# Optimization experiments

Hardware: AMD Instinct MI355X
Metric: run time of the kernel (lower is better)

## Reference

```python
import jax, jax.numpy as jnp
import numpy as np


def setup_inputs() -> dict:
    key = jax.random.key(0)
    ks = jax.random.split(key, 8)
    B, T, H, Hu = 128, 64, 1024, 512
    MJW = 64                    # max_jump_width
    J = 2 * MJW + 1             # size_jump_width_set_nn = 129
    N = 2 * T                   # HMM states (word states + null states)
    I = 64                      # source sentence length
    sc = 0.02
    return {
        "y_hidden": jax.random.normal(ks[0], (B, T, H), jnp.float32),
        # emission probs p(source word i | state s), strictly positive for log
        "emission": jax.random.uniform(ks[1], (B, N, I), jnp.float32, 1e-4, 1.0),
        "source_lengths": jax.random.randint(ks[2], (B,), 1, I + 1),
        "W1": jax.random.normal(ks[3], (H, Hu), jnp.float32) * sc,
        "b1": jnp.zeros((Hu,), jnp.float32),
        "W2": jax.random.normal(ks[4], (Hu, J), jnp.float32) * sc,
        "b2": jnp.zeros((J,), jnp.float32),
        "W3": jax.random.normal(ks[5], (Hu, 1), jnp.float32) * sc,
        "b3": jnp.zeros((1,), jnp.float32),
        "max_jump_width": MJW,
    }


def _build_transition(y_hidden, W1, b1, W2, b2, W3, b3, mjw):
    # Dense(tanh) -> Dense softmax jump-width distribution + Dense sigmoid p0
    B, T, _ = y_hidden.shape
    ts = jnp.tanh(y_hidden @ W1 + b1)                       # [B,T,Hu]
    jw = jax.nn.softmax(ts @ W2 + b2, axis=-1)              # [B,T,J]
    p0 = jax.nn.sigmoid(jnp.squeeze(ts @ W3 + b3, -1))      # [B,T]
    r = jnp.arange(T)
    # banded gather: transition[i, j] = jw[i, mjw + j - i]
    band_idx = mjw + r[None, :] - r[:, None]                # [T,T], in [0, J)
    band = jnp.take_along_axis(jw, band_idx[None], axis=2)  # [B,T,T]
    diag_p0 = jnp.eye(T, dtype=jw.dtype) * p0[:, :, None]   # [B,T,T]
    top = jnp.concatenate([band, diag_p0], axis=2)          # [B,T,2T]
    return jnp.concatenate([top, top], axis=1)              # [B,2T,2T]


def _forward_alignment(transition, emission, source_lengths):
    # Faithful translation of the tf.scan forward algorithm. tf.scan with no
    # initializer uses elems[0] as the initial accumulator and emits it as
    # output[0] (log part = ones, so the [0,0] element is 1.0).
    B, N, I = emission.shape
    em = jnp.transpose(emission, (2, 0, 1))                 # [I,B,N]
    alpha0 = jnp.broadcast_to(em[0][:, None, :], (B, N, N)) # rows all equal e_0
    L0 = jnp.ones((B,), emission.dtype)

    def step(carry, e):
        alpha, L = carry                                    # [B,N,N], [B]
        yi = e[:, None, :]                                  # rows of yi_prob identical
        m1 = jnp.matmul(alpha, transition)                  # [B,N,N]
        tmp = m1 * yi
        tmp = tmp / jnp.sum(tmp, axis=2, keepdims=True)     # row-normalized alpha
        m2 = jnp.matmul(transition, alpha) * yi             # [B,N,N]
        max_j = jnp.max(m2, axis=-1)[:, 0]                  # gather row 0 -> [B]
        state_prev = jnp.sum(m1, axis=1)                    # [B,N]
        state = jnp.log(e) + jnp.log(state_prev) - max_j[:, None]
        state_log = jnp.log(jnp.sum(jnp.exp(state), axis=-1))
        L_new = L + state_log + max_j                       # [B]
        return (tmp, L_new), L_new

    (_, _), logs = jax.lax.scan(step, (alpha0, L0), em[1:])  # [I-1,B]
    logs = jnp.concatenate([L0[None], logs], axis=0).T       # [B,I]
    idx = (source_lengths - 1)[:, None]
    return jnp.take_along_axis(logs, idx, axis=1)[:, 0]      # [B]


def reference(y_hidden, emission, source_lengths, W1, b1, W2, b2, W3, b3, max_jump_width):
    transition = _build_transition(y_hidden, W1, b1, W2, b2, W3, b3, max_jump_width)
    return _forward_alignment(transition, emission, source_lengths)
```

## Files before the change

kernel.cpp:

```cpp
#include <hip/hip_runtime.h>
#include <hip/hip_bf16.h>

typedef float f32x4 __attribute__((ext_vector_type(4)));
typedef __bf16 bf16x8 __attribute__((ext_vector_type(8)));
typedef unsigned short u16;

#define OFF_W1T  0u
#define OFF_W23B 1048576u
#define OFF_TS   1196032u
#define OFF_JWT  9584640u
#define OFF_P0   11681792u

static __device__ __forceinline__ u16 f2bf(float x) {
    __bf16 h = (__bf16)x;
    return __builtin_bit_cast(u16, h);
}

__device__ __forceinline__ void gload16(const void* g, void* l) {
    __builtin_amdgcn_global_load_lds(
        (const __attribute__((address_space(1))) void*)g,
        (__attribute__((address_space(3))) void*)l,
        16, 0, 0);
}

__global__ __launch_bounds__(256) void prep_kernel(
    const float* __restrict__ W1, const float* __restrict__ W2,
    const float* __restrict__ W3,
    __bf16* __restrict__ W1T, __bf16* __restrict__ W23B)
{
    const int t = threadIdx.x;
    if (blockIdx.x < 128) {
        __shared__ __bf16 lds_t[64][72];
        const int kt = blockIdx.x >> 3, nt = blockIdx.x & 7;
        const int k0 = kt * 64, n0 = nt * 64;
        {
            const int kr = t >> 2, c0 = (t & 3) * 16;
            const float* src = W1 + (size_t)(k0 + kr) * 512 + n0 + c0;
            #pragma unroll
            for (int q = 0; q < 4; ++q) {
                float4 v = *(const float4*)(src + q * 4);
                lds_t[kr][c0 + q * 4 + 0] = (__bf16)v.x;
                lds_t[kr][c0 + q * 4 + 1] = (__bf16)v.y;
                lds_t[kr][c0 + q * 4 + 2] = (__bf16)v.z;
                lds_t[kr][c0 + q * 4 + 3] = (__bf16)v.w;
            }
        }
        __syncthreads();
        {
            const int nr = t >> 2, kc = (t & 3) * 16;
            bf16x8 o0, o1;
            #pragma unroll
            for (int j = 0; j < 8; ++j) o0[j] = lds_t[kc + j][nr];
            #pragma unroll
            for (int j = 0; j < 8; ++j) o1[j] = lds_t[kc + 8 + j][nr];
            __bf16* dst = W1T + (size_t)(n0 + nr) * 1024 + k0 + kc;
            *(bf16x8*)(dst)     = o0;
            *(bf16x8*)(dst + 8) = o1;
        }
    } else {
        int g = (blockIdx.x - 128) * 256 + t;
        if (g < 9216) {
            int n = g >> 6;
            int k8 = (g & 63) * 8;
            bf16x8 v;
            #pragma unroll
            for (int j = 0; j < 8; ++j) {
                int k = k8 + j;
                float x = 0.0f;
                if (n < 129) x = W2[(size_t)k * 129 + n];
                else if (n == 129) x = W3[k];
                v[j] = (__bf16)x;
            }
            int kk = k8 >> 5, lg = (k8 >> 3) & 3, ct = n >> 4, lr = n & 15;
            *(bf16x8*)&W23B[(((size_t)(kk * 9 + ct)) * 64 + lg * 16 + lr) * 8] = v;
        }
    }
}

__global__ __launch_bounds__(256, 3) void gemm1_kernel(
    const float* __restrict__ Y, const __bf16* __restrict__ W1T,
    const float* __restrict__ b1, u16* __restrict__ ts)
{
    __shared__ float  As[3][64 * 32];
    __shared__ __bf16 Bs[3][128 * 32];
    const int tid = threadIdx.x;
    const int bid = blockIdx.x;
    const int half = bid >> 8;
    const int b8 = bid & 255;
    const int xcd = b8 & 7;
    const int ii = b8 >> 3;
    const int rb = half * 64 + xcd * 8 + (ii >> 2);
    const int tb = ii & 3;
    const int m0 = rb * 64, n0 = tb * 128;
    const int wid = tid >> 6, lane = tid & 63;
    const int wr = wid >> 1, wc = wid & 1;
    const int lr = lane & 15, lg = lane >> 4;
    const int al = lane >> 3;
    const int au = (lane & 7) ^ al;
    const float* yA0 = Y + (size_t)(m0 + (wid * 2 + 0) * 8 + al) * 1024 + au * 4;
    const float* yA1 = Y + (size_t)(m0 + (wid * 2 + 1) * 8 + al) * 1024 + au * 4;
    const int bl = lane >> 2;
    const int bu = (lane & 3) ^ ((bl >> 1) & 3);
    const __bf16* wB0 = W1T + (size_t)(n0 + (wid * 2 + 0) * 16 + bl) * 1024 + bu * 8;
    const __bf16* wB1 = W1T + (size_t)(n0 + (wid * 2 + 1) * 16 + bl) * 1024 + bu * 8;

    f32x4 acc[2][4];
    #pragma unroll
    for (int m = 0; m < 2; m++)
        #pragma unroll
        for (int n = 0; n < 4; n++) { f32x4 z = {0.f,0.f,0.f,0.f}; acc[m][n] = z; }

#define STAGE(buf, kt) do { \
    gload16(yA0 + (kt) * 32, &As[buf][(wid * 2 + 0) * 256]); \
    gload16(yA1 + (kt) * 32, &As[buf][(wid * 2 + 1) * 256]); \
    gload16(wB0 + (kt) * 32, &Bs[buf][(wid * 2 + 0) * 512]); \
    gload16(wB1 + (kt) * 32, &Bs[buf][(wid * 2 + 1) * 512]); \
} while (0)

#define COMPUTE(buf) do { \
    bf16x8 af[2]; bf16x8 bfr[4]; \
    _Pragma("unroll") \
    for (int m = 0; m < 2; ++m) { \
        const int row = wr * 32 + m * 16 + lr; \
        const int r7 = row & 7; \
        float4 h0 = *(const float4*)&As[buf][row * 32 + (((lg * 2 + 0) ^ r7) * 4)]; \
        float4 h1 = *(const float4*)&As[buf][row * 32 + (((lg * 2 + 1) ^ r7) * 4)]; \
        bf16x8 tt; \
        tt[0]=(__bf16)h0.x; tt[1]=(__bf16)h0.y; tt[2]=(__bf16)h0.z; tt[3]=(__bf16)h0.w; \
        tt[4]=(__bf16)h1.x; tt[5]=(__bf16)h1.y; tt[6]=(__bf16)h1.z; tt[7]=(__bf16)h1.w; \
        af[m] = tt; \
    } \
    _Pragma("unroll") \
    for (int n = 0; n < 4; ++n) { \
        const int rowb = wc * 64 + n * 16 + lr; \
        bfr[n] = *(const bf16x8*)&Bs[buf][rowb * 32 + ((lg ^ ((rowb >> 1) & 3)) * 8)]; \
    } \
    __builtin_amdgcn_s_setprio(1); \
    _Pragma("unroll") \
    for (int m = 0; m < 2; ++m) \
        _Pragma("unroll") \
        for (int n = 0; n < 4; ++n) \
            acc[m][n] = __builtin_amdgcn_mfma_f32_16x16x32_bf16(af[m], bfr[n], acc[m][n], 0, 0, 0); \
    __builtin_amdgcn_s_setprio(0); \
} while (0)

    STAGE(0, 0); STAGE(1, 1);
    {
        int buf = 0, sbuf = 2;
        #pragma unroll 1
        for (int kt = 0; kt < 30; ++kt) {
            asm volatile("s_waitcnt vmcnt(4)" ::: "memory");
            __builtin_amdgcn_s_barrier();
            COMPUTE(buf);
            STAGE(sbuf, kt + 2);
            buf  = (buf  == 2) ? 0 : buf  + 1;
            sbuf = (sbuf == 2) ? 0 : sbuf + 1;
        }
    }
    asm volatile("s_waitcnt vmcnt(4)" ::: "memory");
    __builtin_amdgcn_s_barrier();
    COMPUTE(0);
    asm volatile("s_waitcnt vmcnt(0)" ::: "memory");
    __builtin_amdgcn_s_barrier();
    COMPUTE(1);

    #pragma unroll
    for (int m = 0; m < 2; m++) {
        #pragma unroll
        for (int n = 0; n < 4; n++) {
            int col = n0 + wc * 64 + n * 16 + lr;
            float bias = b1[col];
            #pragma unroll
            for (int j = 0; j < 4; j++) {
                int row = m0 + wr * 32 + m * 16 + lg * 4 + j;
                float v = tanhf(acc[m][n][j] + bias);
                ts[(size_t)row * 512 + col] = f2bf(v);
            }
        }
    }
#undef STAGE
#undef COMPUTE
}

__global__ __launch_bounds__(256) void band_kernel(
    const u16* __restrict__ ts, const u16* __restrict__ W23B,
    const float* __restrict__ b2, const float* __restrict__ b3,
    float* __restrict__ jwT, float* __restrict__ p0)
{
    const int b = blockIdx.x;
    const int tid = threadIdx.x;
    const int w = tid >> 6, lane = tid & 63;
    const int lr = lane & 15, lg = lane >> 4;
    const int r0 = b * 64 + w * 16;

    f32x4 acc[9];
    #pragma unroll
    for (int ct = 0; ct < 9; ct++) { f32x4 z = {0.f,0.f,0.f,0.f}; acc[ct] = z; }

    #pragma unroll 4
    for (int kk = 0; kk < 16; ++kk) {
        bf16x8 a = *(const bf16x8*)(ts + (size_t)(r0 + lr) * 512 + kk * 32 + lg * 8);
        #pragma unroll
        for (int ct = 0; ct < 9; ct++) {
            bf16x8 bv = *(const bf16x8*)(W23B + ((size_t)(kk * 9 + ct) * 64 + lane) * 8);
            acc[ct] = __builtin_amdgcn_mfma_f32_16x16x32_bf16(a, bv, acc[ct], 0, 0, 0);
        }
    }

    float b3v = b3[0];
    #pragma unroll
    for (int j = 0; j < 4; j++) {
        int rloc = w * 16 + lg * 4 + j;
        float v[9];
        float mx = -1e30f;
        #pragma unroll
        for (int ct = 0; ct < 9; ct++) {
            int col = ct * 16 + lr;
            if (col < 129) { float x = acc[ct][j] + b2[col]; v[ct] = x; mx = fmaxf(mx, x); }
            else v[ct] = -1e30f;
        }
        #pragma unroll
        for (int o = 1; o < 16; o <<= 1) mx = fmaxf(mx, __shfl_xor(mx, o));
        float sum = 0.f;
        #pragma unroll
        for (int ct = 0; ct < 9; ct++) {
            int col = ct * 16 + lr;
            if (col < 129) { float e = expf(v[ct] - mx); v[ct] = e; sum += e; }
        }
        #pragma unroll
        for (int o = 1; o < 16; o <<= 1) sum += __shfl_xor(sum, o);
        float inv = 1.0f / sum;
        #pragma unroll
        for (int ct = 0; ct < 9; ct++) {
            int col = ct * 16 + lr;
            int cc = col - 64 + rloc;
            if (col < 129 && cc >= 0 && cc < 64)
                jwT[((size_t)b * 64 + cc) * 64 + rloc] = v[ct] * inv;
        }
        if (lr == 1) {
            float pv = acc[8][j] + b3v;
            p0[b * 64 + rloc] = 1.0f / (1.0f + expf(-pv));
        }
    }
}

__global__ __launch_bounds__(64, 1) void recur_kernel(
    const float* __restrict__ jwT, const float* __restrict__ p0g,
    const float* __restrict__ em, const int* __restrict__ slen,
    float* __restrict__ out)
{
    __shared__ float em_s[128][65];
    __shared__ f32x4 a_bc4[16];
    const int b = blockIdx.x, c = threadIdx.x;

    const float* bb = jwT + ((size_t)b * 64 + c) * 64;
    f32x4 B0  = *(const f32x4*)(bb + 0);
    f32x4 B1  = *(const f32x4*)(bb + 4);
    f32x4 B2  = *(const f32x4*)(bb + 8);
    f32x4 B3  = *(const f32x4*)(bb + 12);
    f32x4 B4  = *(const f32x4*)(bb + 16);
    f32x4 B5  = *(const f32x4*)(bb + 20);
    f32x4 B6  = *(const f32x4*)(bb + 24);
    f32x4 B7  = *(const f32x4*)(bb + 28);
    f32x4 B8  = *(const f32x4*)(bb + 32);
    f32x4 B9  = *(const f32x4*)(bb + 36);
    f32x4 B10 = *(const f32x4*)(bb + 40);
    f32x4 B11 = *(const f32x4*)(bb + 44);
    f32x4 B12 = *(const f32x4*)(bb + 48);
    f32x4 B13 = *(const f32x4*)(bb + 52);
    f32x4 B14 = *(const f32x4*)(bb + 56);
    f32x4 B15 = *(const f32x4*)(bb + 60);

    {
        const float4* eg = (const float4*)(em + (size_t)b * 8192);
        #pragma unroll 8
        for (int q = 0; q < 32; ++q) {
            int i4 = c + q * 64;
            float4 v = eg[i4];
            int base = i4 * 4; int n = base >> 6; int ii = base & 63;
            em_s[n][ii] = v.x; em_s[n][ii + 1] = v.y; em_s[n][ii + 2] = v.z; em_s[n][ii + 3] = v.w;
        }
    }
    const float p0r = p0g[b * 64 + c];
    const int idx = slen[b] - 1;
    __syncthreads();

    float ut = em_s[c][0] + em_s[c + 64][0];
    int Eacc = 0;

    unsigned rbase = (unsigned)(uintptr_t)(__attribute__((address_space(3))) void*)&a_bc4[0];
    unsigned waddr = rbase + (unsigned)c * 4u;
    unsigned emlo_base = (unsigned)(uintptr_t)(__attribute__((address_space(3))) void*)&em_s[c][0];
    unsigned emhi_base = (unsigned)(uintptr_t)(__attribute__((address_space(3))) void*)&em_s[c + 64][0];

    float em_lo = em_s[c][1];
    float em_hi = em_s[c + 64][1];

    #pragma unroll 1
    for (int i = 1; i <= idx; ++i) {
        unsigned ealo = emlo_base + (unsigned)((i + 1) * 4);
        unsigned eahi = emhi_base + (unsigned)((i + 1) * 4);
        f32x4 A0,A1,A2,A3,A4,A5,A6,A7,A8,A9,A10,A11,A12,A13,A14,A15;
        float nlo, nhi;
        asm volatile(
            "ds_write_b32 %19, %18\n\t"
            "ds_read_b128 %0, %20 offset:0\n\t"
            "ds_read_b128 %1, %20 offset:16\n\t"
            "ds_read_b128 %2, %20 offset:32\n\t"
            "ds_read_b128 %3, %20 offset:48\n\t"
            "ds_read_b128 %4, %20 offset:64\n\t"
            "ds_read_b128 %5, %20 offset:80\n\t"
            "ds_read_b128 %6, %20 offset:96\n\t"
            "ds_read_b128 %7, %20 offset:112\n\t"
            "ds_read_b128 %8, %20 offset:128\n\t"
            "ds_read_b128 %9, %20 offset:144\n\t"
            "ds_read_b128 %10, %20 offset:160\n\t"
            "ds_read_b128 %11, %20 offset:176\n\t"
            "ds_read_b128 %12, %20 offset:192\n\t"
            "ds_read_b128 %13, %20 offset:208\n\t"
            "ds_read_b128 %14, %20 offset:224\n\t"
            "ds_read_b128 %15, %20 offset:240\n\t"
            "ds_read_b32 %16, %21\n\t"
            "ds_read_b32 %17, %22"
            : "=&v"(A0), "=&v"(A1), "=&v"(A2),  "=&v"(A3),
              "=&v"(A4), "=&v"(A5), "=&v"(A6),  "=&v"(A7),
              "=&v"(A8), "=&v"(A9), "=&v"(A10), "=&v"(A11),
              "=&v"(A12),"=&v"(A13),"=&v"(A14), "=&v"(A15),
              "=&v"(nlo), "=&v"(nhi)
            : "v"(ut), "v"(waddr), "v"(rbase), "v"(ealo), "v"(eahi)
            : "memory");
        int bits = __builtin_amdgcn_readfirstlane(__float_as_int(ut));
        int ef = (bits >> 23) & 255;
        Eacc += ef - 127;
        float scale = __int_as_float((254 - ef) << 23);
        float emlo_eff = em_lo * scale;
        float emhi_eff = em_hi * p0r * scale;
        asm volatile("s_waitcnt lgkmcnt(0)" ::: "memory");
        __builtin_amdgcn_sched_barrier(0);
        f32x4 va = A0 * B0;
        f32x4 vb = A1 * B1;
        f32x4 vc = A2 * B2;
        f32x4 vd = A3 * B3;
        va = va + A4 * B4;   vb = vb + A5 * B5;
        vc = vc + A6 * B6;   vd = vd + A7 * B7;
        va = va + A8 * B8;   vb = vb + A9 * B9;
        vc = vc + A10 * B10; vd = vd + A11 * B11;
        va = va + A12 * B12; vb = vb + A13 * B13;
        vc = vc + A14 * B14; vd = vd + A15 * B15;
        f32x4 vs = (va + vb) + (vc + vd);
        float sum = (vs[0] + vs[1]) + (vs[2] + vs[3]);
        ut = sum * emlo_eff + ut * emhi_eff;
        em_lo = nlo; em_hi = nhi;
    }
    float r = ut;
    #pragma unroll
    for (int o = 1; o < 64; o <<= 1) r += __shfl_xor(r, o);
    if (c == 0) {
        float res = 1.0f;
        if (idx > 0)
            res = 1.0f + 0.6931471805599453f * ((float)Eacc + __log2f(r) + 7.0f * (float)idx);
        out[b] = res;
    }
}

extern "C" void kernel_launch(void* const* d_in, const int* in_sizes, int n_in,
                              void* d_out, int out_size, void* d_ws, size_t ws_size,
                              hipStream_t stream)
{
    const float* Y   = (const float*)d_in[0];
    const float* em  = (const float*)d_in[1];
    const int*   sl  = (const int*)d_in[2];
    const float* W1  = (const float*)d_in[3];
    const float* b1  = (const float*)d_in[4];
    const float* W2  = (const float*)d_in[5];
    const float* b2  = (const float*)d_in[6];
    const float* W3  = (const float*)d_in[7];
    const float* b3  = (const float*)d_in[8];
    float* out = (float*)d_out;
    char* ws = (char*)d_ws;

    __bf16* W1T  = (__bf16*)(ws + OFF_W1T);
    __bf16* W23B = (__bf16*)(ws + OFF_W23B);
    u16*    ts   = (u16*)(ws + OFF_TS);
    float*  jwT  = (float*)(ws + OFF_JWT);
    float*  p0   = (float*)(ws + OFF_P0);

    prep_kernel<<<164, 256, 0, stream>>>(W1, W2, W3, W1T, W23B);
    gemm1_kernel<<<512, 256, 0, stream>>>(Y, W1T, b1, ts);
    band_kernel<<<128, 256, 0, stream>>>(ts, (const u16*)W23B, b2, b3, jwT, p0);
    recur_kernel<<<128, 64, 0, stream>>>(jwT, p0, em, sl, out);
}
```

Before: 76.17 us.

## Replace sequential vector recurrence with bf16 MFMA matrix-product scan

The per-batch recurrence kernel, which walked a 64-element state vector through idx serial matvec steps on one wavefront, is replaced by a 256-thread kernel. This kernel accumulates the product of per-step 64x64 transition matrices with bf16 MFMA, using swizzled LDS tiles and max-based exponent rescaling. The final vector is applied once at the end. The aim is to use matrix cores and four waves in place of a latency-bound single-wave loop, but each step now does a full matrix-matrix product plus a block barrier. Keeping the products in bf16 also risks losing accuracy.

```diff
diff --git a/kernel.cpp b/kernel.cpp
--- a/kernel.cpp
+++ b/kernel.cpp
@@ -3,6 +3,7 @@
 
 typedef float f32x4 __attribute__((ext_vector_type(4)));
 typedef __bf16 bf16x8 __attribute__((ext_vector_type(8)));
+typedef __bf16 bf16x4 __attribute__((ext_vector_type(4)));
 typedef unsigned short u16;
 
 #define OFF_W1T  0u
@@ -244,122 +245,167 @@
     }
 }
 
-__global__ __launch_bounds__(64, 1) void recur_kernel(
+__global__ __launch_bounds__(256, 1) void scan_kernel(
     const float* __restrict__ jwT, const float* __restrict__ p0g,
     const float* __restrict__ em, const int* __restrict__ slen,
     float* __restrict__ out)
 {
-    __shared__ float em_s[128][65];
-    __shared__ f32x4 a_bc4[16];
-    const int b = blockIdx.x, c = threadIdx.x;
-
-    const float* bb = jwT + ((size_t)b * 64 + c) * 64;
-    f32x4 B0  = *(const f32x4*)(bb + 0);
-    f32x4 B1  = *(const f32x4*)(bb + 4);
-    f32x4 B2  = *(const f32x4*)(bb + 8);
-    f32x4 B3  = *(const f32x4*)(bb + 12);
-    f32x4 B4  = *(const f32x4*)(bb + 16);
-    f32x4 B5  = *(const f32x4*)(bb + 20);
-    f32x4 B6  = *(const f32x4*)(bb + 24);
-    f32x4 B7  = *(const f32x4*)(bb + 28);
-    f32x4 B8  = *(const f32x4*)(bb + 32);
-    f32x4 B9  = *(const f32x4*)(bb + 36);
-    f32x4 B10 = *(const f32x4*)(bb + 40);
-    f32x4 B11 = *(const f32x4*)(bb + 44);
-    f32x4 B12 = *(const f32x4*)(bb + 48);
-    f32x4 B13 = *(const f32x4*)(bb + 52);
-    f32x4 B14 = *(const f32x4*)(bb + 56);
-    f32x4 B15 = *(const f32x4*)(bb + 60);
+    __shared__ __bf16 Mb[64 * 64];
+    __shared__ __bf16 PT[2][64 * 64];
+    __shared__ float  emT[64][132];
+    __shared__ float  p0s[64];
+    __shared__ float  wmax[2][4];
+    __shared__ float  partial[4][64];
+
+    const int b = blockIdx.x;
+    const int t = threadIdx.x;
+    const int w = t >> 6, lane = t & 63;
+    const int lr = lane & 15, lg = lane >> 4;
+    const int idx = slen[b] - 1;
+
+    if (idx <= 0) { if (t == 0) out[b] = 1.0f; return; }
 
     {
-        const float4* eg = (const float4*)(em + (size_t)b * 8192);
-        #pragma unroll 8
-        for (int q = 0; q < 32; ++q) {
-            int i4 = c + q * 64;
-            float4 v = eg[i4];
-            int base = i4 * 4; int n = base >> 6; int ii = base & 63;
-            em_s[n][ii] = v.x; em_s[n][ii + 1] = v.y; em_s[n][ii + 2] = v.z; em_s[n][ii + 3] = v.w;
-        }
-    }
-    const float p0r = p0g[b * 64 + c];
-    const int idx = slen[b] - 1;
+        const float4* mg4 = (const float4*)(jwT + (size_t)b * 4096);
+        #pragma unroll
+        for (int q = 0; q < 4; ++q) {
+            int i4 = t + q * 256;
+            float4 v = mg4[i4];
+            int m = i4 >> 4, k0 = (i4 & 15) * 4;
+            int u = (k0 >> 3) ^ (m & 7);
+            bf16x4 o; o[0]=(__bf16)v.x; o[1]=(__bf16)v.y; o[2]=(__bf16)v.z; o[3]=(__bf16)v.w;
+            *(bf16x4*)&Mb[m * 64 + u * 8 + (k0 & 7)] = o;
+        }
+        const float4* eg4 = (const float4*)(em + (size_t)b * 8192);
+        #pragma unroll
+        for (int q = 0; q < 8; ++q) {
+            int i4 = t + q * 256;
+            float4 v = eg4[i4];
+            int n = i4 >> 4, i0 = (i4 & 15) * 4;
+            emT[i0 + 0][n] = v.x;
+            emT[i0 + 1][n] = v.y;
+            emT[i0 + 2][n] = v.z;
+            emT[i0 + 3][n] = v.w;
+        }
+        if (t < 64) p0s[t] = p0g[b * 64 + t];
+    }
     __syncthreads();
 
-    float ut = em_s[c][0] + em_s[c + 64][0];
+    const int m = w * 16 + lr;
+    const float p0r = p0s[m];
+
+    {
+        int n = lane;
+        float lmax0 = 0.f;
+        #pragma unroll
+        for (int mg = 0; mg < 4; ++mg) {
+            int m4 = w * 16 + mg * 4;
+            bf16x4 o;
+            #pragma unroll
+            for (int j = 0; j < 4; ++j) {
+                int mm = m4 + j;
+                float g = emT[1][mm] *
+                    (float)Mb[mm * 64 + (((n >> 3) ^ (mm & 7)) * 8) + (n & 7)];
+                if (n == mm) g += emT[1][mm + 64] * p0s[mm];
+                lmax0 = fmaxf(lmax0, g);
+                o[j] = (__bf16)g;
+            }
+            int u = (m4 >> 3) ^ (n & 7);
+            *(bf16x4*)&PT[0][n * 64 + u * 8 + (m4 & 7)] = o;
+        }
+        #pragma unroll
+        for (int o2 = 1; o2 < 64; o2 <<= 1) lmax0 = fmaxf(lmax0, __shfl_xor(lmax0, o2));
+        if (lane == 0) wmax[0][w] = lmax0;
+    }
+    __syncthreads();
+
     int Eacc = 0;
-
-    unsigned rbase = (unsigned)(uintptr_t)(__attribute__((address_space(3))) void*)&a_bc4[0];
-    unsigned waddr = rbase + (unsigned)c * 4u;
-    unsigned emlo_base = (unsigned)(uintptr_t)(__attribute__((address_space(3))) void*)&em_s[c][0];
-    unsigned emhi_base = (unsigned)(uintptr_t)(__attribute__((address_space(3))) void*)&em_s[c + 64][0];
-
-    float em_lo = em_s[c][1];
-    float em_hi = em_s[c + 64][1];
-
+    int cur = 0;
     #pragma unroll 1
-    for (int i = 1; i <= idx; ++i) {
-        unsigned ealo = emlo_base + (unsigned)((i + 1) * 4);
-        unsigned eahi = emhi_base + (unsigned)((i + 1) * 4);
-        f32x4 A0,A1,A2,A3,A4,A5,A6,A7,A8,A9,A10,A11,A12,A13,A14,A15;
-        float nlo, nhi;
-        asm volatile(
-            "ds_write_b32 %19, %18\n\t"
-            "ds_read_b128 %0, %20 offset:0\n\t"
-            "ds_read_b128 %1, %20 offset:16\n\t"
-            "ds_read_b128 %2, %20 offset:32\n\t"
-            "ds_read_b128 %3, %20 offset:48\n\t"
-            "ds_read_b128 %4, %20 offset:64\n\t"
-            "ds_read_b128 %5, %20 offset:80\n\t"
-            "ds_read_b128 %6, %20 offset:96\n\t"
-            "ds_read_b128 %7, %20 offset:112\n\t"
-            "ds_read_b128 %8, %20 offset:128\n\t"
-            "ds_read_b128 %9, %20 offset:144\n\t"
-            "ds_read_b128 %10, %20 offset:160\n\t"
-            "ds_read_b128 %11, %20 offset:176\n\t"
-            "ds_read_b128 %12, %20 offset:192\n\t"
-            "ds_read_b128 %13, %20 offset:208\n\t"
-            "ds_read_b128 %14, %20 offset:224\n\t"
-            "ds_read_b128 %15, %20 offset:240\n\t"
-            "ds_read_b32 %16, %21\n\t"
-            "ds_read_b32 %17, %22"
-            : "=&v"(A0), "=&v"(A1), "=&v"(A2),  "=&v"(A3),
-              "=&v"(A4), "=&v"(A5), "=&v"(A6),  "=&v"(A7),
-              "=&v"(A8), "=&v"(A9), "=&v"(A10), "=&v"(A11),
-              "=&v"(A12),"=&v"(A13),"=&v"(A14), "=&v"(A15),
-              "=&v"(nlo), "=&v"(nhi)
-            : "v"(ut), "v"(waddr), "v"(rbase), "v"(ealo), "v"(eahi)
-            : "memory");
-        int bits = __builtin_amdgcn_readfirstlane(__float_as_int(ut));
-        int ef = (bits >> 23) & 255;
-        Eacc += ef - 127;
-        float scale = __int_as_float((254 - ef) << 23);
-        float emlo_eff = em_lo * scale;
-        float emhi_eff = em_hi * p0r * scale;
-        asm volatile("s_waitcnt lgkmcnt(0)" ::: "memory");
-        __builtin_amdgcn_sched_barrier(0);
-        f32x4 va = A0 * B0;
-        f32x4 vb = A1 * B1;
-        f32x4 vc = A2 * B2;
-        f32x4 vd = A3 * B3;
-        va = va + A4 * B4;   vb = vb + A5 * B5;
-        vc = vc + A6 * B6;   vd = vd + A7 * B7;
-        va = va + A8 * B8;   vb = vb + A9 * B9;
-        vc = vc + A10 * B10; vd = vd + A11 * B11;
-        va = va + A12 * B12; vb = vb + A13 * B13;
-        vc = vc + A14 * B14; vd = vd + A15 * B15;
-        f32x4 vs = (va + vb) + (vc + vd);
-        float sum = (vs[0] + vs[1]) + (vs[2] + vs[3]);
-        ut = sum * emlo_eff + ut * emhi_eff;
-        em_lo = nlo; em_hi = nhi;
-    }
-    float r = ut;
-    #pragma unroll
-    for (int o = 1; o < 64; o <<= 1) r += __shfl_xor(r, o);
-    if (c == 0) {
-        float res = 1.0f;
-        if (idx > 0)
-            res = 1.0f + 0.6931471805599453f * ((float)Eacc + __log2f(r) + 7.0f * (float)idx);
-        out[b] = res;
+    for (int i = 2; i <= idx; ++i) {
+        const int rp = i & 1, wp = rp ^ 1;
+        float mx = fmaxf(fmaxf(wmax[rp][0], wmax[rp][1]),
+                         fmaxf(wmax[rp][2], wmax[rp][3]));
+        int E = ((__float_as_int(mx) >> 23) & 255) - 127;
+        Eacc += E;
+        float scale = __int_as_float((127 - E) << 23);
+        float emlo_eff = emT[i][m] * scale;
+        float emhi_eff = emT[i][m + 64] * p0r * scale;
+
+        bf16x8 afr[2];
+        #pragma unroll
+        for (int kk = 0; kk < 2; ++kk) {
+            int kbase = kk * 32 + lg * 8;
+            int u = (kbase >> 3) ^ (m & 7);
+            bf16x8 mv = *(const bf16x8*)&Mb[m * 64 + u * 8];
+            bf16x8 aa;
+            #pragma unroll
+            for (int j = 0; j < 8; ++j) {
+                float h = (float)mv[j] * emlo_eff;
+                if (m - kbase == j) h += emhi_eff;
+                aa[j] = (__bf16)h;
+            }
+            afr[kk] = aa;
+        }
+        f32x4 acc[4];
+        #pragma unroll
+        for (int ct = 0; ct < 4; ++ct) { f32x4 z = {0.f,0.f,0.f,0.f}; acc[ct] = z; }
+        #pragma unroll
+        for (int kk = 0; kk < 2; ++kk) {
+            int kbase = kk * 32 + lg * 8;
+            #pragma unroll
+            for (int ct = 0; ct < 4; ++ct) {
+                int row = ct * 16 + lr;
+                int u = (kbase >> 3) ^ (row & 7);
+                bf16x8 bv = *(const bf16x8*)&PT[cur][row * 64 + u * 8];
+                acc[ct] = __builtin_amdgcn_mfma_f32_16x16x32_bf16(afr[kk], bv, acc[ct], 0, 0, 0);
+            }
+        }
+        float lm = 0.f;
+        #pragma unroll
+        for (int ct = 0; ct < 4; ++ct)
+            #pragma unroll
+            for (int j = 0; j < 4; ++j) lm = fmaxf(lm, acc[ct][j]);
+        #pragma unroll
+        for (int o2 = 1; o2 < 64; o2 <<= 1) lm = fmaxf(lm, __shfl_xor(lm, o2));
+        if (lane == 0) wmax[wp][w] = lm;
+        int m4 = w * 16 + lg * 4;
+        #pragma unroll
+        for (int ct = 0; ct < 4; ++ct) {
+            int row = ct * 16 + lr;
+            bf16x4 o;
+            #pragma unroll
+            for (int j = 0; j < 4; ++j) o[j] = (__bf16)acc[ct][j];
+            int u = (m4 >> 3) ^ (row & 7);
+            *(bf16x4*)&PT[cur ^ 1][row * 64 + u * 8 + (m4 & 7)] = o;
+        }
+        __syncthreads();
+        cur ^= 1;
+    }
+
+    {
+        int c = lane;
+        float s = 0.f;
+        #pragma unroll
+        for (int mg = 0; mg < 4; ++mg) {
+            int m4 = w * 16 + mg * 4;
+            int u = (m4 >> 3) ^ (c & 7);
+            bf16x4 v4 = *(const bf16x4*)&PT[cur][c * 64 + u * 8 + (m4 & 7)];
+            s += (float)v4[0] + (float)v4[1] + (float)v4[2] + (float)v4[3];
+        }
+        partial[w][c] = s;
+    }
+    __syncthreads();
+    if (w == 0) {
+        int c = lane;
+        float tot = partial[0][c] + partial[1][c] + partial[2][c] + partial[3][c];
+        float a0c = emT[0][c] + emT[0][c + 64];
+        float v = tot * a0c;
+        #pragma unroll
+        for (int o2 = 1; o2 < 64; o2 <<= 1) v += __shfl_xor(v, o2);
+        if (c == 0)
+            out[b] = 1.0f + 0.6931471805599453f *
+                     ((float)Eacc + __log2f(v) + 7.0f * (float)idx);
     }
 }
 
@@ -388,5 +434,5 @@
     prep_kernel<<<164, 256, 0, stream>>>(W1, W2, W3, W1T, W23B);
     gemm1_kernel<<<512, 256, 0, stream>>>(Y, W1T, b1, ts);
     band_kernel<<<128, 256, 0, stream>>>(ts, (const u16*)W23B, b2, b3, jwT, p0);
-    recur_kernel<<<128, 64, 0, stream>>>(jwT, p0, em, sl, out);
-}
+    scan_kernel<<<128, 256, 0, stream>>>(jwT, p0, em, sl, out);
+}
```

New measurement: 104.6 us. 1.37x slower.
